# Optimization experiments

Hardware: AMD Instinct MI355X
Metric: run time of the kernel (lower is better)

The kernel has to match this reference:

```python
import jax, jax.numpy as jnp
import numpy as np


def _lstm(x, W_ih, W_hh, b_ih, b_hh):
    """PyTorch-semantics LSTM over [B, T, F] -> [B, T, H]. Gate order: i, f, g, o."""
    H = W_hh.shape[1]
    # Precompute input projection for all timesteps: [B, T, 4H]
    xg = jnp.einsum('btf,gf->btg', x, W_ih) + b_ih + b_hh
    xg = jnp.transpose(xg, (1, 0, 2))  # time-major [T, B, 4H]
    B = x.shape[0]
    h0 = jnp.zeros((B, H), dtype=x.dtype)
    c0 = jnp.zeros((B, H), dtype=x.dtype)

    def step(carry, xt):
        h, c = carry
        gates = xt + h @ W_hh.T  # [B, 4H]
        i, f, g, o = jnp.split(gates, 4, axis=-1)
        i = jax.nn.sigmoid(i)
        f = jax.nn.sigmoid(f)
        g = jnp.tanh(g)
        o = jax.nn.sigmoid(o)
        c = f * c + i * g
        h = o * jnp.tanh(c)
        return (h, c), h

    _, hs = jax.lax.scan(step, (h0, c0), xg)
    return jnp.transpose(hs, (1, 0, 2))  # [B, T, H]


def setup_inputs() -> dict:
    key = jax.random.key(0)
    ks = jax.random.split(key, 16)
    B, T, F = 4096, 256, 32
    H1, H2, D1 = 64, 32, 16
    s1 = 1.0 / np.sqrt(H1)
    s2 = 1.0 / np.sqrt(H2)
    inp = {
        'x': jax.random.normal(ks[0], (B, T, F), dtype=jnp.float32),
        'W_ih1': jax.random.uniform(ks[1], (4 * H1, F), jnp.float32, -s1, s1),
        'W_hh1': jax.random.uniform(ks[2], (4 * H1, H1), jnp.float32, -s1, s1),
        'b_ih1': jax.random.uniform(ks[3], (4 * H1,), jnp.float32, -s1, s1),
        'b_hh1': jax.random.uniform(ks[4], (4 * H1,), jnp.float32, -s1, s1),
        'W_ih2': jax.random.uniform(ks[5], (4 * H2, H1), jnp.float32, -s2, s2),
        'W_hh2': jax.random.uniform(ks[6], (4 * H2, H2), jnp.float32, -s2, s2),
        'b_ih2': jax.random.uniform(ks[7], (4 * H2,), jnp.float32, -s2, s2),
        'b_hh2': jax.random.uniform(ks[8], (4 * H2,), jnp.float32, -s2, s2),
        'W_fc1': jax.random.uniform(ks[9], (D1, H2), jnp.float32, -s2, s2),
        'b_fc1': jax.random.uniform(ks[10], (D1,), jnp.float32, -s2, s2),
        'W_fc2': jax.random.uniform(ks[11], (1, D1), jnp.float32, -0.25, 0.25),
        'b_fc2': jax.random.uniform(ks[12], (1,), jnp.float32, -0.25, 0.25),
    }
    return inp


def reference(x, W_ih1, W_hh1, b_ih1, b_hh1, W_ih2, W_hh2, b_ih2, b_hh2,
              W_fc1, b_fc1, W_fc2, b_fc2):
    # Dropout is identity in eval/inference mode.
    h = _lstm(x, W_ih1, W_hh1, b_ih1, b_hh1)        # [B, T, 64]
    h = _lstm(h, W_ih2, W_hh2, b_ih2, b_hh2)        # [B, T, 32]
    h = h[:, -1, :]                                  # [B, 32]
    h = jax.nn.relu(h @ W_fc1.T + b_fc1)             # [B, 16]
    out = h @ W_fc2.T + b_fc2                        # [B, 1]
    return out.squeeze(-1)                           # [B]
```

## Files before the change

### kernel.cpp

```cpp
#include <hip/hip_runtime.h>

#define T_   256
#define F_   32
#define NBB  16
#define TPB  768
#define IMW  104
#define XLW  40
#define PR1  260
#define PR2  132

typedef __attribute__((ext_vector_type(8))) short bf16x8;
typedef __attribute__((ext_vector_type(4))) float f32x4;

#define K1f  (-1.44269504f)
#define K2f  (-2.88539008f)

__device__ __forceinline__ unsigned short bf16_rne(float x){
    unsigned u = __float_as_uint(x);
    u += 0x7FFF + ((u >> 16) & 1);
    return (unsigned short)(u >> 16);
}
__device__ __forceinline__ void bf16_split(float x, unsigned short& h, unsigned short& l){
    h = bf16_rne(x);
    float xr = __uint_as_float(((unsigned)h) << 16);
    l = bf16_rne(x - xr);
}
__device__ __forceinline__ void make_frags_s(const float* __restrict__ p8, float s,
                                             bf16x8& fh, bf16x8& fl){
    #pragma unroll
    for (int e = 0; e < 8; ++e){
        unsigned short h, l; bf16_split(s * p8[e], h, l);
        fh[e] = (short)h; fl[e] = (short)l;
    }
}
__device__ __forceinline__ float sigm_pre(float p){
    return __builtin_amdgcn_rcpf(1.f + __builtin_amdgcn_exp2f(p));
}
__device__ __forceinline__ float tanh_pre(float p){
    return fmaf(2.f, __builtin_amdgcn_rcpf(1.f + __builtin_amdgcn_exp2f(p)), -1.f);
}
__device__ __forceinline__ float unit_combine(float gi, float gf, float gg, float go, float& c){
    const float i_ = sigm_pre(gi);
    const float f_ = sigm_pre(gf);
    const float g_ = tanh_pre(gg);
    const float o_ = sigm_pre(go);
    c = fmaf(f_, c, i_ * g_);
    return o_ * tanh_pre(K2f * c);
}

#define MFMA(A,B,C) __builtin_amdgcn_mfma_f32_16x16x32_bf16((A),(B),(C),0,0,0)

__device__ __forceinline__ void step_barrier(){
    asm volatile("s_waitcnt lgkmcnt(0)" ::: "memory");
    __builtin_amdgcn_s_barrier();
}

__global__ __launch_bounds__(TPB, 3) void lstm_mfma(
    const float* __restrict__ x,
    const float* __restrict__ W_ih1,
    const float* __restrict__ W_hh1,
    const float* __restrict__ b_ih1,
    const float* __restrict__ b_hh1,
    const float* __restrict__ W_ih2,
    const float* __restrict__ W_hh2,
    const float* __restrict__ b_ih2,
    const float* __restrict__ b_hh2,
    const float* __restrict__ W_fc1,
    const float* __restrict__ b_fc1,
    const float* __restrict__ W_fc2,
    const float* __restrict__ b_fc2,
    float* __restrict__ out)
{
    const int tid  = threadIdx.x;
    const int lane = tid & 63;
    const int wid  = tid >> 6;
    const int bb   = lane & 15;
    const int kg   = (lane >> 4) & 3;
    const int b0   = blockIdx.x * NBB;

    __shared__ __align__(16) unsigned short i1h[2][NBB][IMW];
    __shared__ __align__(16) unsigned short x1l[2][NBB][XLW];
    __shared__ __align__(16) unsigned short i2h[2][NBB][IMW];
    __shared__ __align__(16) float pre1[NBB * PR1];
    __shared__ __align__(16) float pre2[NBB * PR2];
    __shared__ float hfin[NBB][32];
    __shared__ float hd[NBB][16];

    bf16x8 wh[2][3], wl[2][3];
    f32x4  bfr[2];
    int    offs[2];
    if (wid < 8){
        #pragma unroll
        for (int tt = 0; tt < 2; ++tt){
            const int Tt = 2*wid + tt;
            const int g = Tt >> 2, rb = Tt & 3;
            const float s = (g == 2) ? K2f : K1f;
            offs[tt] = 64*g + 16*rb;
            const int r = offs[tt] + bb;
            make_frags_s(&W_ih1[r*32 +      8*kg], s, wh[tt][0], wl[tt][0]);
            make_frags_s(&W_hh1[r*64 +      8*kg], s, wh[tt][1], wl[tt][1]);
            make_frags_s(&W_hh1[r*64 + 32 + 8*kg], s, wh[tt][2], wl[tt][2]);
            #pragma unroll
            for (int q = 0; q < 4; ++q){
                const int row = offs[tt] + 4*kg + q;
                bfr[tt][q] = s * (b_ih1[row] + b_hh1[row]);
            }
        }
    } else {
        const int j = wid - 8;
        #pragma unroll
        for (int tt = 0; tt < 2; ++tt){
            const int St = 2*j + tt;
            const int g = St >> 1, rb = St & 1;
            const float s = (g == 2) ? K2f : K1f;
            offs[tt] = 32*g + 16*rb;
            const int r = offs[tt] + bb;
            make_frags_s(&W_ih2[r*64 +      8*kg], s, wh[tt][0], wl[tt][0]);
            make_frags_s(&W_ih2[r*64 + 32 + 8*kg], s, wh[tt][1], wl[tt][1]);
            make_frags_s(&W_hh2[r*32 +      8*kg], s, wh[tt][2], wl[tt][2]);
            #pragma unroll
            for (int q = 0; q < 4; ++q){
                const int row = offs[tt] + 4*kg + q;
                bfr[tt][q] = s * (b_ih2[row] + b_hh2[row]);
            }
        }
    }

    const int cb = tid >> 5;
    const int u0 = (tid & 31) * 2;
    float c1a = 0.f, c1b = 0.f;
    const int lt  = tid & 255;
    const int cb2 = lt >> 4;
    const int v0  = (lt & 15) * 2;
    float c2a = 0.f, c2b = 0.f;
    const int xf = (lt & 15) * 2;
    const size_t xbase = (size_t)(b0 + cb2) * (T_*F_) + xf;
    float2 xc = make_float2(0.f, 0.f);

    for (int i = tid; i < 2*NBB*IMW; i += TPB){
        (&i1h[0][0][0])[i] = 0; (&i2h[0][0][0])[i] = 0;
    }
    for (int i = tid; i < 2*NBB*XLW; i += TPB) (&x1l[0][0][0])[i] = 0;
    __syncthreads();
    if (wid >= 8){
        float2 x0 = *(const float2*)&x[xbase];
        unsigned short h0h, h0l, h1h, h1l;
        bf16_split(x0.x, h0h, h0l); bf16_split(x0.y, h1h, h1l);
        *(unsigned*)&i1h[0][cb2][xf] = (unsigned)h0h | ((unsigned)h1h << 16);
        *(unsigned*)&x1l[0][cb2][xf] = (unsigned)h0l | ((unsigned)h1l << 16);
        xc = *(const float2*)&x[xbase + F_];
    }
    __syncthreads();

    for (int t = 0; t <= T_ + 1; ++t){
        const int cur = t & 1, nxt = cur ^ 1;

        if (wid < 8){
            if (t < T_){
                const unsigned short* ph = &i1h[cur][0][0] + bb*IMW + 8*kg;
                bf16x8 vh[3];
                #pragma unroll
                for (int kb = 0; kb < 3; ++kb)
                    vh[kb] = *(const bf16x8*)(ph + 32*kb);
                const bf16x8 vl0 = *(const bf16x8*)&x1l[cur][bb][8*kg];
                __builtin_amdgcn_s_setprio(1);
                f32x4 a0 = bfr[0], a1 = bfr[1];
                #pragma unroll
                for (int kb = 0; kb < 3; ++kb){
                    a0 = MFMA(wh[0][kb], vh[kb], a0);
                    a1 = MFMA(wh[1][kb], vh[kb], a1);
                }
                #pragma unroll
                for (int kb = 0; kb < 3; ++kb){
                    a0 = MFMA(wl[0][kb], vh[kb], a0);
                    a1 = MFMA(wl[1][kb], vh[kb], a1);
                }
                a0 = MFMA(wh[0][0], vl0, a0);
                a1 = MFMA(wh[1][0], vl0, a1);
                __builtin_amdgcn_s_setprio(0);
                *(f32x4*)&pre1[bb*PR1 + offs[0] + 4*kg] = a0;
                *(f32x4*)&pre1[bb*PR1 + offs[1] + 4*kg] = a1;
            }
        } else {
            const int m = t - 2;
            if (m >= 0 && m < T_){
                const float* p = &pre2[cb2*PR2];
                const float2 gi = *(const float2*)&p[     v0];
                const float2 gf = *(const float2*)&p[32 + v0];
                const float2 gg = *(const float2*)&p[64 + v0];
                const float2 go = *(const float2*)&p[96 + v0];
                const float h0 = unit_combine(gi.x, gf.x, gg.x, go.x, c2a);
                const float h1 = unit_combine(gi.y, gf.y, gg.y, go.y, c2b);
                *(unsigned*)&i2h[nxt][cb2][64 + v0] =
                    (unsigned)bf16_rne(h0) | ((unsigned)bf16_rne(h1) << 16);
                if (m == T_ - 1){ hfin[cb2][v0] = h0; hfin[cb2][v0+1] = h1; }
            }
            if (t + 1 < T_){
                unsigned short h0h, h0l, h1h, h1l;
                bf16_split(xc.x, h0h, h0l); bf16_split(xc.y, h1h, h1l);
                *(unsigned*)&i1h[nxt][cb2][xf] = (unsigned)h0h | ((unsigned)h1h << 16);
                *(unsigned*)&x1l[nxt][cb2][xf] = (unsigned)h0l | ((unsigned)h1l << 16);
                const int tn = (t + 2 < T_) ? t + 2 : T_ - 1;
                xc = *(const float2*)&x[xbase + (size_t)tn * F_];
            }
        }
        step_barrier();

        if (wid < 8){
            if (t < T_){
                const float* p = &pre1[cb*PR1];
                const float2 gi = *(const float2*)&p[      u0];
                const float2 gf = *(const float2*)&p[ 64 + u0];
                const float2 gg = *(const float2*)&p[128 + u0];
                const float2 go = *(const float2*)&p[192 + u0];
                const float h0 = unit_combine(gi.x, gf.x, gg.x, go.x, c1a);
                const float h1 = unit_combine(gi.y, gf.y, gg.y, go.y, c1b);
                const unsigned wh_ =
                    (unsigned)bf16_rne(h0) | ((unsigned)bf16_rne(h1) << 16);
                *(unsigned*)&i1h[nxt][cb][32 + u0] = wh_;
                *(unsigned*)&i2h[cur][cb][u0]      = wh_;
            }
        } else {
            const int k = t - 1;
            if (k >= 0 && k < T_){
                const unsigned short* ph = &i2h[nxt][0][0] + bb*IMW + 8*kg;
                bf16x8 vh[3];
                #pragma unroll
                for (int kb = 0; kb < 3; ++kb)
                    vh[kb] = *(const bf16x8*)(ph + 32*kb);
                __builtin_amdgcn_s_setprio(1);
                f32x4 a0 = bfr[0], a1 = bfr[1];
                #pragma unroll
                for (int kb = 0; kb < 3; ++kb){
                    a0 = MFMA(wh[0][kb], vh[kb], a0);
                    a1 = MFMA(wh[1][kb], vh[kb], a1);
                }
                #pragma unroll
                for (int kb = 0; kb < 3; ++kb){
                    a0 = MFMA(wl[0][kb], vh[kb], a0);
                    a1 = MFMA(wl[1][kb], vh[kb], a1);
                }
                __builtin_amdgcn_s_setprio(0);
                *(f32x4*)&pre2[bb*PR2 + offs[0] + 4*kg] = a0;
                *(f32x4*)&pre2[bb*PR2 + offs[1] + 4*kg] = a1;
            }
        }
        step_barrier();
    }

    __syncthreads();
    if (tid < NBB * 16){
        const int b = tid >> 4, j2 = tid & 15;
        float a = b_fc1[j2];
        #pragma unroll
        for (int kk = 0; kk < 32; ++kk) a = fmaf(W_fc1[j2*32 + kk], hfin[b][kk], a);
        hd[b][j2] = fmaxf(a, 0.f);
    }
    __syncthreads();
    if (tid < NBB){
        float a = b_fc2[0];
        #pragma unroll
        for (int kk = 0; kk < 16; ++kk) a = fmaf(W_fc2[kk], hd[tid][kk], a);
        out[b0 + tid] = a;
    }
}

extern "C" void kernel_launch(void* const* d_in, const int* in_sizes, int n_in,
                              void* d_out, int out_size, void* d_ws, size_t ws_size,
                              hipStream_t stream) {
    const float* x     = (const float*)d_in[0];
    const float* W_ih1 = (const float*)d_in[1];
    const float* W_hh1 = (const float*)d_in[2];
    const float* b_ih1 = (const float*)d_in[3];
    const float* b_hh1 = (const float*)d_in[4];
    const float* W_ih2 = (const float*)d_in[5];
    const float* W_hh2 = (const float*)d_in[6];
    const float* b_ih2 = (const float*)d_in[7];
    const float* b_hh2 = (const float*)d_in[8];
    const float* W_fc1 = (const float*)d_in[9];
    const float* b_fc1 = (const float*)d_in[10];
    const float* W_fc2 = (const float*)d_in[11];
    const float* b_fc2 = (const float*)d_in[12];
    float* out = (float*)d_out;

    const int B = in_sizes[0] / (T_ * F_);
    dim3 grid(B / NBB), block(TPB);
    hipLaunchKernelGGL(lstm_mfma, grid, block, 0, stream,
                       x, W_ih1, W_hh1, b_ih1, b_hh1,
                       W_ih2, W_hh2, b_ih2, b_hh2,
                       W_fc1, b_fc1, W_fc2, b_fc2, out);
}
```

Before: 244.8 us.

## Specialize warps into MFMA and elementwise roles with four tiles per MFMA warp

Reassigns the 12 waves so that 4 waves do all layer-1 MFMA tiles (4 tiles each), 2 waves do layer-2 MFMA, 4 waves do layer-1 gate combination plus x staging, and 2 waves do layer-2 gate combination. Before, every wave did both MFMA and elementwise work. The aim is to let MFMA and transcendental work from different waves overlap within each phase, and to vectorize the combines to 4 units per thread. In exchange, the MFMA waves hold twice as many weight fragments in registers and carry longer dependent MFMA chains per step.

```diff
diff --git a/kernel.cpp b/kernel.cpp
--- a/kernel.cpp
+++ b/kernel.cpp
@@ -11,6 +11,7 @@
 
 typedef __attribute__((ext_vector_type(8))) short bf16x8;
 typedef __attribute__((ext_vector_type(4))) float f32x4;
+typedef __attribute__((ext_vector_type(4))) unsigned short ush4;
 
 #define K1f  (-1.44269504f)
 #define K2f  (-2.88539008f)
@@ -86,16 +87,14 @@
     __shared__ float hfin[NBB][32];
     __shared__ float hd[NBB][16];
 
-    bf16x8 wh[2][3], wl[2][3];
-    f32x4  bfr[2];
-    int    offs[2];
-    if (wid < 8){
+    bf16x8 wh[4][3], wl[4][3];
+    f32x4  bfr[4];
+    int    offs[4];
+    if (wid < 4){
+        const float s = (wid == 2) ? K2f : K1f;
         #pragma unroll
-        for (int tt = 0; tt < 2; ++tt){
-            const int Tt = 2*wid + tt;
-            const int g = Tt >> 2, rb = Tt & 3;
-            const float s = (g == 2) ? K2f : K1f;
-            offs[tt] = 64*g + 16*rb;
+        for (int tt = 0; tt < 4; ++tt){
+            offs[tt] = 64*wid + 16*tt;
             const int r = offs[tt] + bb;
             make_frags_s(&W_ih1[r*32 +      8*kg], s, wh[tt][0], wl[tt][0]);
             make_frags_s(&W_hh1[r*64 +      8*kg], s, wh[tt][1], wl[tt][1]);
@@ -106,14 +105,13 @@
                 bfr[tt][q] = s * (b_ih1[row] + b_hh1[row]);
             }
         }
-    } else {
-        const int j = wid - 8;
+    } else if (wid < 6){
+        const int j = wid - 4;
         #pragma unroll
-        for (int tt = 0; tt < 2; ++tt){
-            const int St = 2*j + tt;
-            const int g = St >> 1, rb = St & 1;
+        for (int tt = 0; tt < 4; ++tt){
+            const int g = 2*j + (tt >> 1);
             const float s = (g == 2) ? K2f : K1f;
-            offs[tt] = 32*g + 16*rb;
+            offs[tt] = 64*j + 16*tt;
             const int r = offs[tt] + bb;
             make_frags_s(&W_ih2[r*64 +      8*kg], s, wh[tt][0], wl[tt][0]);
             make_frags_s(&W_ih2[r*64 + 32 + 8*kg], s, wh[tt][1], wl[tt][1]);
@@ -126,28 +124,29 @@
         }
     }
 
-    const int cb = tid >> 5;
-    const int u0 = (tid & 31) * 2;
-    float c1a = 0.f, c1b = 0.f;
-    const int lt  = tid & 255;
-    const int cb2 = lt >> 4;
-    const int v0  = (lt & 15) * 2;
-    float c2a = 0.f, c2b = 0.f;
-    const int xf = (lt & 15) * 2;
-    const size_t xbase = (size_t)(b0 + cb2) * (T_*F_) + xf;
+    const int ct = tid - 384;
+    const int cb = (ct >> 4) & 15;
+    const int u0 = (ct & 15) * 4;
+    float c1[4] = {0.f, 0.f, 0.f, 0.f};
+    const int xf = (ct & 15) * 2;
+    const size_t xbase = (size_t)(b0 + cb) * (T_*F_) + xf;
     float2 xc = make_float2(0.f, 0.f);
+    const int c2t = tid - 640;
+    const int cb2 = (c2t >> 3) & 15;
+    const int v0  = (c2t & 7) * 4;
+    float c2[4] = {0.f, 0.f, 0.f, 0.f};
 
     for (int i = tid; i < 2*NBB*IMW; i += TPB){
         (&i1h[0][0][0])[i] = 0; (&i2h[0][0][0])[i] = 0;
     }
     for (int i = tid; i < 2*NBB*XLW; i += TPB) (&x1l[0][0][0])[i] = 0;
     __syncthreads();
-    if (wid >= 8){
+    if (wid >= 6 && wid < 10){
         float2 x0 = *(const float2*)&x[xbase];
         unsigned short h0h, h0l, h1h, h1l;
         bf16_split(x0.x, h0h, h0l); bf16_split(x0.y, h1h, h1l);
-        *(unsigned*)&i1h[0][cb2][xf] = (unsigned)h0h | ((unsigned)h1h << 16);
-        *(unsigned*)&x1l[0][cb2][xf] = (unsigned)h0l | ((unsigned)h1l << 16);
+        *(unsigned*)&i1h[0][cb][xf] = (unsigned)h0h | ((unsigned)h1h << 16);
+        *(unsigned*)&x1l[0][cb][xf] = (unsigned)h0l | ((unsigned)h1l << 16);
         xc = *(const float2*)&x[xbase + F_];
     }
     __syncthreads();
@@ -155,7 +154,7 @@
     for (int t = 0; t <= T_ + 1; ++t){
         const int cur = t & 1, nxt = cur ^ 1;
 
-        if (wid < 8){
+        if (wid < 4){
             if (t < T_){
                 const unsigned short* ph = &i1h[cur][0][0] + bb*IMW + 8*kg;
                 bf16x8 vh[3];
@@ -164,63 +163,64 @@
                     vh[kb] = *(const bf16x8*)(ph + 32*kb);
                 const bf16x8 vl0 = *(const bf16x8*)&x1l[cur][bb][8*kg];
                 __builtin_amdgcn_s_setprio(1);
-                f32x4 a0 = bfr[0], a1 = bfr[1];
+                f32x4 a0 = bfr[0], a1 = bfr[1], a2 = bfr[2], a3 = bfr[3];
                 #pragma unroll
                 for (int kb = 0; kb < 3; ++kb){
                     a0 = MFMA(wh[0][kb], vh[kb], a0);
                     a1 = MFMA(wh[1][kb], vh[kb], a1);
+                    a2 = MFMA(wh[2][kb], vh[kb], a2);
+                    a3 = MFMA(wh[3][kb], vh[kb], a3);
                 }
                 #pragma unroll
                 for (int kb = 0; kb < 3; ++kb){
                     a0 = MFMA(wl[0][kb], vh[kb], a0);
                     a1 = MFMA(wl[1][kb], vh[kb], a1);
+                    a2 = MFMA(wl[2][kb], vh[kb], a2);
+                    a3 = MFMA(wl[3][kb], vh[kb], a3);
                 }
                 a0 = MFMA(wh[0][0], vl0, a0);
                 a1 = MFMA(wh[1][0], vl0, a1);
+                a2 = MFMA(wh[2][0], vl0, a2);
+                a3 = MFMA(wh[3][0], vl0, a3);
                 __builtin_amdgcn_s_setprio(0);
                 *(f32x4*)&pre1[bb*PR1 + offs[0] + 4*kg] = a0;
                 *(f32x4*)&pre1[bb*PR1 + offs[1] + 4*kg] = a1;
-            }
-        } else {
+                *(f32x4*)&pre1[bb*PR1 + offs[2] + 4*kg] = a2;
+                *(f32x4*)&pre1[bb*PR1 + offs[3] + 4*kg] = a3;
+            }
+        } else if (wid >= 10){
             const int m = t - 2;
             if (m >= 0 && m < T_){
                 const float* p = &pre2[cb2*PR2];
-                const float2 gi = *(const float2*)&p[     v0];
-                const float2 gf = *(const float2*)&p[32 + v0];
-                const float2 gg = *(const float2*)&p[64 + v0];
-                const float2 go = *(const float2*)&p[96 + v0];
-                const float h0 = unit_combine(gi.x, gf.x, gg.x, go.x, c2a);
-                const float h1 = unit_combine(gi.y, gf.y, gg.y, go.y, c2b);
-                *(unsigned*)&i2h[nxt][cb2][64 + v0] =
-                    (unsigned)bf16_rne(h0) | ((unsigned)bf16_rne(h1) << 16);
-                if (m == T_ - 1){ hfin[cb2][v0] = h0; hfin[cb2][v0+1] = h1; }
-            }
+                const f32x4 gi = *(const f32x4*)&p[     v0];
+                const f32x4 gf = *(const f32x4*)&p[32 + v0];
+                const f32x4 gg = *(const f32x4*)&p[64 + v0];
+                const f32x4 go = *(const f32x4*)&p[96 + v0];
+                ush4 HH;
+                float hv[4];
+                #pragma unroll
+                for (int q = 0; q < 4; ++q){
+                    hv[q] = unit_combine(gi[q], gf[q], gg[q], go[q], c2[q]);
+                    HH[q] = bf16_rne(hv[q]);
+                }
+                *(ush4*)&i2h[nxt][cb2][64 + v0] = HH;
+                if (m == T_ - 1){
+                    *(f32x4*)&hfin[cb2][v0] = *(f32x4*)hv;
+                }
+            }
+        } else if (wid >= 6){
             if (t + 1 < T_){
                 unsigned short h0h, h0l, h1h, h1l;
                 bf16_split(xc.x, h0h, h0l); bf16_split(xc.y, h1h, h1l);
-                *(unsigned*)&i1h[nxt][cb2][xf] = (unsigned)h0h | ((unsigned)h1h << 16);
-                *(unsigned*)&x1l[nxt][cb2][xf] = (unsigned)h0l | ((unsigned)h1l << 16);
+                *(unsigned*)&i1h[nxt][cb][xf] = (unsigned)h0h | ((unsigned)h1h << 16);
+                *(unsigned*)&x1l[nxt][cb][xf] = (unsigned)h0l | ((unsigned)h1l << 16);
                 const int tn = (t + 2 < T_) ? t + 2 : T_ - 1;
                 xc = *(const float2*)&x[xbase + (size_t)tn * F_];
             }
         }
         step_barrier();
 
-        if (wid < 8){
-            if (t < T_){
-                const float* p = &pre1[cb*PR1];
-                const float2 gi = *(const float2*)&p[      u0];
-                const float2 gf = *(const float2*)&p[ 64 + u0];
-                const float2 gg = *(const float2*)&p[128 + u0];
-                const float2 go = *(const float2*)&p[192 + u0];
-                const float h0 = unit_combine(gi.x, gf.x, gg.x, go.x, c1a);
-                const float h1 = unit_combine(gi.y, gf.y, gg.y, go.y, c1b);
-                const unsigned wh_ =
-                    (unsigned)bf16_rne(h0) | ((unsigned)bf16_rne(h1) << 16);
-                *(unsigned*)&i1h[nxt][cb][32 + u0] = wh_;
-                *(unsigned*)&i2h[cur][cb][u0]      = wh_;
-            }
-        } else {
+        if (wid >= 4 && wid < 6){
             const int k = t - 1;
             if (k >= 0 && k < T_){
                 const unsigned short* ph = &i2h[nxt][0][0] + bb*IMW + 8*kg;
@@ -229,20 +229,42 @@
                 for (int kb = 0; kb < 3; ++kb)
                     vh[kb] = *(const bf16x8*)(ph + 32*kb);
                 __builtin_amdgcn_s_setprio(1);
-                f32x4 a0 = bfr[0], a1 = bfr[1];
+                f32x4 a0 = bfr[0], a1 = bfr[1], a2 = bfr[2], a3 = bfr[3];
                 #pragma unroll
                 for (int kb = 0; kb < 3; ++kb){
                     a0 = MFMA(wh[0][kb], vh[kb], a0);
                     a1 = MFMA(wh[1][kb], vh[kb], a1);
+                    a2 = MFMA(wh[2][kb], vh[kb], a2);
+                    a3 = MFMA(wh[3][kb], vh[kb], a3);
                 }
                 #pragma unroll
                 for (int kb = 0; kb < 3; ++kb){
                     a0 = MFMA(wl[0][kb], vh[kb], a0);
                     a1 = MFMA(wl[1][kb], vh[kb], a1);
+                    a2 = MFMA(wl[2][kb], vh[kb], a2);
+                    a3 = MFMA(wl[3][kb], vh[kb], a3);
                 }
                 __builtin_amdgcn_s_setprio(0);
                 *(f32x4*)&pre2[bb*PR2 + offs[0] + 4*kg] = a0;
                 *(f32x4*)&pre2[bb*PR2 + offs[1] + 4*kg] = a1;
+                *(f32x4*)&pre2[bb*PR2 + offs[2] + 4*kg] = a2;
+                *(f32x4*)&pre2[bb*PR2 + offs[3] + 4*kg] = a3;
+            }
+        } else if (wid >= 6 && wid < 10){
+            if (t < T_){
+                const float* p = &pre1[cb*PR1];
+                const f32x4 gi = *(const f32x4*)&p[      u0];
+                const f32x4 gf = *(const f32x4*)&p[ 64 + u0];
+                const f32x4 gg = *(const f32x4*)&p[128 + u0];
+                const f32x4 go = *(const f32x4*)&p[192 + u0];
+                ush4 HH;
+                #pragma unroll
+                for (int q = 0; q < 4; ++q){
+                    const float h = unit_combine(gi[q], gf[q], gg[q], go[q], c1[q]);
+                    HH[q] = bf16_rne(h);
+                }
+                *(ush4*)&i1h[nxt][cb][32 + u0] = HH;
+                *(ush4*)&i2h[cur][cb][u0]      = HH;
             }
         }
         step_barrier();
```

Result: slower. 398.1 us (+62.7%).

## Spread layer-2 LSTM work across 8 waves using a 1024-thread block

Applied to the files above, without the earlier changes.

Raises the block to 1024 threads, so layer 2 runs on 8 waves instead of 4. Each layer-2 wave now computes one 16-row gate tile (6 MFMAs instead of 12), and each layer-2 thread handles one hidden unit and one x element instead of two. The goal is to shorten the per-step critical path of the layer-2 phase that sits between the barriers. The cost is fewer resident blocks per CU: the waves-per-EU hint changes from the earlier 3-blocks bound, so occupancy and register budget shift, and 16-bit LDS stores replace 32-bit ones.

```diff
diff --git a/kernel.cpp b/kernel.cpp
--- a/kernel.cpp
+++ b/kernel.cpp
@@ -3,7 +3,7 @@
 #define T_   256
 #define F_   32
 #define NBB  16
-#define TPB  768
+#define TPB  1024
 #define IMW  104
 #define XLW  40
 #define PR1  260
@@ -55,7 +55,8 @@
     __builtin_amdgcn_s_barrier();
 }
 
-__global__ __launch_bounds__(TPB, 3) void lstm_mfma(
+__global__ __launch_bounds__(TPB) __attribute__((amdgpu_waves_per_eu(4, 4)))
+void lstm_mfma(
     const float* __restrict__ x,
     const float* __restrict__ W_ih1,
     const float* __restrict__ W_hh1,
@@ -108,34 +109,29 @@
         }
     } else {
         const int j = wid - 8;
-        #pragma unroll
-        for (int tt = 0; tt < 2; ++tt){
-            const int St = 2*j + tt;
-            const int g = St >> 1, rb = St & 1;
-            const float s = (g == 2) ? K2f : K1f;
-            offs[tt] = 32*g + 16*rb;
-            const int r = offs[tt] + bb;
-            make_frags_s(&W_ih2[r*64 +      8*kg], s, wh[tt][0], wl[tt][0]);
-            make_frags_s(&W_ih2[r*64 + 32 + 8*kg], s, wh[tt][1], wl[tt][1]);
-            make_frags_s(&W_hh2[r*32 +      8*kg], s, wh[tt][2], wl[tt][2]);
-            #pragma unroll
-            for (int q = 0; q < 4; ++q){
-                const int row = offs[tt] + 4*kg + q;
-                bfr[tt][q] = s * (b_ih2[row] + b_hh2[row]);
-            }
+        const int g = j >> 1;
+        const float s = (g == 2) ? K2f : K1f;
+        offs[0] = 32*g + 16*(j & 1);
+        const int r = offs[0] + bb;
+        make_frags_s(&W_ih2[r*64 +      8*kg], s, wh[0][0], wl[0][0]);
+        make_frags_s(&W_ih2[r*64 + 32 + 8*kg], s, wh[0][1], wl[0][1]);
+        make_frags_s(&W_hh2[r*32 +      8*kg], s, wh[0][2], wl[0][2]);
+        #pragma unroll
+        for (int q = 0; q < 4; ++q){
+            const int row = offs[0] + 4*kg + q;
+            bfr[0][q] = s * (b_ih2[row] + b_hh2[row]);
         }
     }
 
     const int cb = tid >> 5;
     const int u0 = (tid & 31) * 2;
     float c1a = 0.f, c1b = 0.f;
-    const int lt  = tid & 255;
-    const int cb2 = lt >> 4;
-    const int v0  = (lt & 15) * 2;
-    float c2a = 0.f, c2b = 0.f;
-    const int xf = (lt & 15) * 2;
-    const size_t xbase = (size_t)(b0 + cb2) * (T_*F_) + xf;
-    float2 xc = make_float2(0.f, 0.f);
+    const int xi  = tid & 511;
+    const int cb2 = xi >> 5;
+    const int v   = xi & 31;
+    float c2 = 0.f;
+    const size_t xbase = (size_t)(b0 + cb2) * (T_*F_) + v;
+    float xc = 0.f;
 
     for (int i = tid; i < 2*NBB*IMW; i += TPB){
         (&i1h[0][0][0])[i] = 0; (&i2h[0][0][0])[i] = 0;
@@ -143,12 +139,10 @@
     for (int i = tid; i < 2*NBB*XLW; i += TPB) (&x1l[0][0][0])[i] = 0;
     __syncthreads();
     if (wid >= 8){
-        float2 x0 = *(const float2*)&x[xbase];
-        unsigned short h0h, h0l, h1h, h1l;
-        bf16_split(x0.x, h0h, h0l); bf16_split(x0.y, h1h, h1l);
-        *(unsigned*)&i1h[0][cb2][xf] = (unsigned)h0h | ((unsigned)h1h << 16);
-        *(unsigned*)&x1l[0][cb2][xf] = (unsigned)h0l | ((unsigned)h1l << 16);
-        xc = *(const float2*)&x[xbase + F_];
+        unsigned short hh, hl;
+        bf16_split(x[xbase], hh, hl);
+        i1h[0][cb2][v] = hh; x1l[0][cb2][v] = hl;
+        xc = x[xbase + F_];
     }
     __syncthreads();
 
@@ -185,23 +179,16 @@
             const int m = t - 2;
             if (m >= 0 && m < T_){
                 const float* p = &pre2[cb2*PR2];
-                const float2 gi = *(const float2*)&p[     v0];
-                const float2 gf = *(const float2*)&p[32 + v0];
-                const float2 gg = *(const float2*)&p[64 + v0];
-                const float2 go = *(const float2*)&p[96 + v0];
-                const float h0 = unit_combine(gi.x, gf.x, gg.x, go.x, c2a);
-                const float h1 = unit_combine(gi.y, gf.y, gg.y, go.y, c2b);
-                *(unsigned*)&i2h[nxt][cb2][64 + v0] =
-                    (unsigned)bf16_rne(h0) | ((unsigned)bf16_rne(h1) << 16);
-                if (m == T_ - 1){ hfin[cb2][v0] = h0; hfin[cb2][v0+1] = h1; }
+                const float h2 = unit_combine(p[v], p[32 + v], p[64 + v], p[96 + v], c2);
+                i2h[nxt][cb2][64 + v] = bf16_rne(h2);
+                if (m == T_ - 1) hfin[cb2][v] = h2;
             }
             if (t + 1 < T_){
-                unsigned short h0h, h0l, h1h, h1l;
-                bf16_split(xc.x, h0h, h0l); bf16_split(xc.y, h1h, h1l);
-                *(unsigned*)&i1h[nxt][cb2][xf] = (unsigned)h0h | ((unsigned)h1h << 16);
-                *(unsigned*)&x1l[nxt][cb2][xf] = (unsigned)h0l | ((unsigned)h1l << 16);
+                unsigned short hh, hl;
+                bf16_split(xc, hh, hl);
+                i1h[nxt][cb2][v] = hh; x1l[nxt][cb2][v] = hl;
                 const int tn = (t + 2 < T_) ? t + 2 : T_ - 1;
-                xc = *(const float2*)&x[xbase + (size_t)tn * F_];
+                xc = x[xbase + (size_t)tn * F_];
             }
         }
         step_barrier();
@@ -229,20 +216,13 @@
                 for (int kb = 0; kb < 3; ++kb)
                     vh[kb] = *(const bf16x8*)(ph + 32*kb);
                 __builtin_amdgcn_s_setprio(1);
-                f32x4 a0 = bfr[0], a1 = bfr[1];
-                #pragma unroll
-                for (int kb = 0; kb < 3; ++kb){
-                    a0 = MFMA(wh[0][kb], vh[kb], a0);
-                    a1 = MFMA(wh[1][kb], vh[kb], a1);
-                }
-                #pragma unroll
-                for (int kb = 0; kb < 3; ++kb){
-                    a0 = MFMA(wl[0][kb], vh[kb], a0);
-                    a1 = MFMA(wl[1][kb], vh[kb], a1);
-                }
+                f32x4 a0 = bfr[0];
+                #pragma unroll
+                for (int kb = 0; kb < 3; ++kb) a0 = MFMA(wh[0][kb], vh[kb], a0);
+                #pragma unroll
+                for (int kb = 0; kb < 3; ++kb) a0 = MFMA(wl[0][kb], vh[kb], a0);
                 __builtin_amdgcn_s_setprio(0);
                 *(f32x4*)&pre2[bb*PR2 + offs[0] + 4*kg] = a0;
-                *(f32x4*)&pre2[bb*PR2 + offs[1] + 4*kg] = a1;
             }
         }
         step_barrier();
```

Measured after the change: 252.9 us. 3.3% more time.
